# Optimization experiments

Hardware: AMD Instinct MI355X
Metric: run time of the kernel (lower is better)

Reference implementation:

```python
import jax, jax.numpy as jnp
import numpy as np

D_MODEL = 512
NUM_HEADS = 8
D_FF = 2048
SEQ = 2048
BATCH = 2
EPS = 1e-5


def _linear(x, W, b):
    # x: [S,B,D_in], W: [D_out, D_in] (torch convention), b: [D_out]
    return jnp.einsum('sbd,ed->sbe', x, W) + b


def _layer_norm(x, g, b):
    mu = jnp.mean(x, axis=-1, keepdims=True)
    var = jnp.var(x, axis=-1, keepdims=True)
    return (x - mu) * jax.lax.rsqrt(var + EPS) * g + b


def _mha(q_in, k_in, v_in, W, b, mask4d, num_heads):
    # q_in: [Sq,B,D], k_in/v_in: [Sk,B,D]; W: [4,D,D], b: [4,D]
    Sq, B, D = q_in.shape
    Sk = k_in.shape[0]
    dk = D // num_heads
    q = _linear(q_in, W[0], b[0]).reshape(Sq, B, num_heads, dk).transpose(1, 2, 0, 3)
    k = _linear(k_in, W[1], b[1]).reshape(Sk, B, num_heads, dk).transpose(1, 2, 0, 3)
    v = _linear(v_in, W[2], b[2]).reshape(Sk, B, num_heads, dk).transpose(1, 2, 0, 3)
    scores = jnp.einsum('bhqd,bhkd->bhqk', q, k) / jnp.sqrt(jnp.asarray(dk, q.dtype))
    scores = jnp.where(mask4d, -jnp.inf, scores)
    p = jax.nn.softmax(scores, axis=-1)  # dropout p=0 -> identity
    o = jnp.einsum('bhqk,bhkd->bhqd', p, v)  # [B,H,Sq,dk]
    o = o.transpose(2, 0, 1, 3).reshape(Sq, B, D)
    return _linear(o, W[3], b[3])


def setup_inputs() -> dict:
    key = jax.random.key(0)
    ks = jax.random.split(key, 12)
    scale = 1.0 / np.sqrt(D_MODEL)
    inp = {
        'x': jax.random.normal(ks[0], (SEQ, BATCH, D_MODEL), jnp.float32),
        'memory': jax.random.normal(ks[1], (SEQ, BATCH, D_MODEL), jnp.float32),
        # causal mask: True = masked (strictly upper triangular)
        'tgt_mask': jnp.triu(jnp.ones((SEQ, SEQ), dtype=bool), k=1),
        # per-batch key padding mask for cross attention
        'memory_mask': jax.random.randint(ks[2], (BATCH, SEQ), 0, 2) > 0,
        'sa_W': jax.random.normal(ks[3], (4, D_MODEL, D_MODEL), jnp.float32) * scale,
        'sa_b': jnp.zeros((4, D_MODEL), jnp.float32),
        'ca_W': jax.random.normal(ks[4], (4, D_MODEL, D_MODEL), jnp.float32) * scale,
        'ca_b': jnp.zeros((4, D_MODEL), jnp.float32),
        'w1': jax.random.normal(ks[5], (D_FF, D_MODEL), jnp.float32) * scale,
        'b1': jnp.zeros((D_FF,), jnp.float32),
        'w2': jax.random.normal(ks[6], (D_MODEL, D_FF), jnp.float32) * (1.0 / np.sqrt(D_FF)),
        'b2': jnp.zeros((D_MODEL,), jnp.float32),
        'ln_g': jnp.ones((3, D_MODEL), jnp.float32),
        'ln_b': jnp.zeros((3, D_MODEL), jnp.float32),
    }
    return inp


def reference(x, memory, tgt_mask, memory_mask, sa_W, sa_b, ca_W, ca_b,
              w1, b1, w2, b2, ln_g, ln_b):
    # self-attention block (pre-norm, residual)
    nx = _layer_norm(x, ln_g[0], ln_b[0])
    sa = _mha(nx, nx, nx, sa_W, sa_b, tgt_mask[None, None], NUM_HEADS)
    x = x + sa
    # cross-attention block
    nx = _layer_norm(x, ln_g[1], ln_b[1])
    ca = _mha(nx, memory, memory, ca_W, ca_b, memory_mask[:, None, None, :], NUM_HEADS)
    x = x + ca
    # FFN block
    nx = _layer_norm(x, ln_g[2], ln_b[2])
    ff = _linear(jax.nn.relu(_linear(nx, w1, b1)), w2, b2)
    return x + ff
```

## Files before the change

kernel.cpp:

```cpp
#include <hip/hip_runtime.h>

#define S_LEN 2048
#define BATCH_N 2
#define DM 512
#define H_N 8
#define DK_N 64
#define FF_N 2048
#define M_TOK (S_LEN*BATCH_N)
#define QSZ (BATCH_N*H_N*S_LEN*DK_N)
#define MN_PART 2097152

typedef __attribute__((ext_vector_type(8))) short short8;
typedef __attribute__((ext_vector_type(4))) float f32x4;
typedef __attribute__((ext_vector_type(16))) float f32x16;
typedef __attribute__((ext_vector_type(4))) unsigned uint4v;

__device__ __forceinline__ unsigned short f2b(float f) {
  union { float f; unsigned u; } v; v.f = f;
  unsigned r = v.u + 0x7FFFu + ((v.u >> 16) & 1u);
  return (unsigned short)(r >> 16);
}
__device__ __forceinline__ float b2f(unsigned short u) {
  union { unsigned u; float f; } v; v.u = ((unsigned)u) << 16; return v.f;
}

__device__ __forceinline__ void gl_lds16(const void* g, void* l) {
  __builtin_amdgcn_global_load_lds(
      (__attribute__((address_space(1))) unsigned int*)(unsigned long long)g,
      (__attribute__((address_space(3))) unsigned int*)(unsigned int)(unsigned long long)l,
      16, 0, 0);
}

__device__ __forceinline__ void cast4(const float* __restrict__ src,
                                      unsigned short* __restrict__ dst, int i) {
  float4 v = *(const float4*)(src + i);
  ushort4 o; o.x = f2b(v.x); o.y = f2b(v.y); o.z = f2b(v.z); o.w = f2b(v.w);
  *(ushort4*)(dst + i) = o;
}

__device__ __forceinline__ void ln_row_wave(const float* __restrict__ in,
    const float* __restrict__ g, const float* __restrict__ b,
    unsigned short* __restrict__ out, int row, int lane) {
  const float4* src = (const float4*)(in + (size_t)row * DM);
  float4 v0 = src[lane*2], v1 = src[lane*2 + 1];
  float s  = v0.x+v0.y+v0.z+v0.w + v1.x+v1.y+v1.z+v1.w;
  float ss = v0.x*v0.x+v0.y*v0.y+v0.z*v0.z+v0.w*v0.w
           + v1.x*v1.x+v1.y*v1.y+v1.z*v1.z+v1.w*v1.w;
  #pragma unroll
  for (int off = 32; off >= 1; off >>= 1) {
    s  += __shfl_xor(s,  off);
    ss += __shfl_xor(ss, off);
  }
  float mean = s * (1.f/512.f);
  float inv  = rsqrtf(ss * (1.f/512.f) - mean*mean + 1e-5f);
  float4 g0 = ((const float4*)g)[lane*2], g1 = ((const float4*)g)[lane*2 + 1];
  float4 b0 = ((const float4*)b)[lane*2], b1 = ((const float4*)b)[lane*2 + 1];
  ushort4 o0, o1;
  o0.x = f2b((v0.x-mean)*inv*g0.x + b0.x);
  o0.y = f2b((v0.y-mean)*inv*g0.y + b0.y);
  o0.z = f2b((v0.z-mean)*inv*g0.z + b0.z);
  o0.w = f2b((v0.w-mean)*inv*g0.w + b0.w);
  o1.x = f2b((v1.x-mean)*inv*g1.x + b1.x);
  o1.y = f2b((v1.y-mean)*inv*g1.y + b1.y);
  o1.z = f2b((v1.z-mean)*inv*g1.z + b1.z);
  o1.w = f2b((v1.w-mean)*inv*g1.w + b1.w);
  ushort4* dst = (ushort4*)(out + (size_t)row * DM);
  dst[lane*2]     = o0;
  dst[lane*2 + 1] = o1;
}

__global__ __launch_bounds__(256) void prep_kernel(
    const float* __restrict__ sa_W, const float* __restrict__ ca_W,
    const float* __restrict__ w1, const float* __restrict__ w2,
    const float* __restrict__ memory, const int* __restrict__ mm,
    const float* __restrict__ x, const float* __restrict__ ln_g,
    const float* __restrict__ ln_b,
    unsigned short* __restrict__ o_sa, unsigned short* __restrict__ o_ca,
    unsigned short* __restrict__ o_w1, unsigned short* __restrict__ o_w2,
    unsigned short* __restrict__ o_mem, unsigned long long* __restrict__ bmo,
    unsigned short* __restrict__ nx)
{
  int blk = blockIdx.x, t = threadIdx.x;
  if (blk < 1024)      cast4(sa_W, o_sa, (blk*256 + t)*4);
  else if (blk < 2048) cast4(ca_W, o_ca, ((blk-1024)*256 + t)*4);
  else if (blk < 3072) cast4(w1,   o_w1, ((blk-2048)*256 + t)*4);
  else if (blk < 4096) cast4(w2,   o_w2, ((blk-3072)*256 + t)*4);
  else if (blk < 6144) cast4(memory, o_mem, ((blk-4096)*256 + t)*4);
  else if (blk == 6144) {
    if (t < 64) {
      int b = t >> 5, kt = t & 31;
      unsigned long long m = 0ull;
      for (int j = 0; j < 64; j++)
        m |= (unsigned long long)(mm[b*S_LEN + kt*64 + j] != 0) << j;
      bmo[b*32 + kt] = m;
    }
  } else {
    int row = (blk - 6145)*4 + (t >> 6);
    ln_row_wave(x, ln_g, ln_b, nx, row, t & 63);
  }
}

__global__ __launch_bounds__(256) void ln4_kernel(const float* __restrict__ in,
                                                  const float* __restrict__ g,
                                                  const float* __restrict__ b,
                                                  unsigned short* __restrict__ out) {
  ln_row_wave(in, g, b, out, blockIdx.x*4 + (threadIdx.x >> 6), threadIdx.x & 63);
}

template<int RELU, int OUTMODE, int RESID>
__global__ __launch_bounds__(256) void gemm_bt(
    const unsigned short* __restrict__ A, const unsigned short* __restrict__ W,
    const float* __restrict__ bias, const float* __restrict__ resid,
    float* __restrict__ Cf, unsigned short* __restrict__ Cb,
    int M, int N, int K, int Kstride)
{
  __shared__ unsigned short As[2][64*40];
  __shared__ unsigned short Bs[2][64*40];
  int tid = threadIdx.x;
  int lane = tid & 63, w = tid >> 6;
  int wr = w >> 1, wc = w & 1;
  int bm = blockIdx.y * 64, bn = blockIdx.x * 64;
  int kz = blockIdx.z;
  f32x4 acc[2][2] = {};
  int lrow = tid >> 2;
  int lcg  = (tid & 3) * 8;
  const size_t aoff = (size_t)(bm + lrow) * Kstride + (size_t)kz * K + lcg;
  const size_t boff = (size_t)(bn + lrow) * Kstride + (size_t)kz * K + lcg;
  int fr = lane & 15, kg = (lane >> 4) * 8;
  short8 pa = *(const short8*)&A[aoff];
  short8 pb = *(const short8*)&W[boff];
  *(short8*)&As[0][lrow*40 + lcg] = pa;
  *(short8*)&Bs[0][lrow*40 + lcg] = pb;
  __syncthreads();
  int cur = 0;
  for (int k0 = 0; k0 < K; k0 += 32) {
    bool hn = (k0 + 32) < K;
    if (hn) {
      pa = *(const short8*)&A[aoff + k0 + 32];
      pb = *(const short8*)&W[boff + k0 + 32];
    }
    short8 af0 = *(const short8*)&As[cur][(wr*32 +      fr)*40 + kg];
    short8 af1 = *(const short8*)&As[cur][(wr*32 + 16 + fr)*40 + kg];
    short8 bf0 = *(const short8*)&Bs[cur][(wc*32 +      fr)*40 + kg];
    short8 bf1 = *(const short8*)&Bs[cur][(wc*32 + 16 + fr)*40 + kg];
    acc[0][0] = __builtin_amdgcn_mfma_f32_16x16x32_bf16(af0, bf0, acc[0][0], 0,0,0);
    acc[0][1] = __builtin_amdgcn_mfma_f32_16x16x32_bf16(af0, bf1, acc[0][1], 0,0,0);
    acc[1][0] = __builtin_amdgcn_mfma_f32_16x16x32_bf16(af1, bf0, acc[1][0], 0,0,0);
    acc[1][1] = __builtin_amdgcn_mfma_f32_16x16x32_bf16(af1, bf1, acc[1][1], 0,0,0);
    if (hn) {
      *(short8*)&As[cur^1][lrow*40 + lcg] = pa;
      *(short8*)&Bs[cur^1][lrow*40 + lcg] = pb;
    }
    __syncthreads();
    cur ^= 1;
  }
  int rbase = (lane >> 4) * 4;
  #pragma unroll
  for (int m = 0; m < 2; m++) {
    #pragma unroll
    for (int n = 0; n < 2; n++) {
      int col = bn + wc*32 + n*16 + (lane & 15);
      float bc = (OUTMODE == 3) ? 0.f : bias[col];
      #pragma unroll
      for (int r = 0; r < 4; r++) {
        int row = bm + wr*32 + m*16 + rbase + r;
        float vv = acc[m][n][r] + bc;
        if (RELU) vv = fmaxf(vv, 0.f);
        if (OUTMODE == 2) {
          int which = col >> 9, hh = (col >> 6) & 7, dd = col & 63;
          size_t idx = ((((size_t)which*BATCH_N + (row & 1))*H_N + hh)*S_LEN + (row >> 1))*DK_N + dd;
          Cb[idx] = f2b(vv);
        } else if (OUTMODE == 3) {
          Cf[(size_t)kz*MN_PART + (size_t)row*N + col] = vv;
        } else {
          size_t idx = (size_t)row * N + col;
          if (RESID) vv += resid[idx];
          if (OUTMODE == 1) Cb[idx] = f2b(vv);
          else              Cf[idx] = vv;
        }
      }
    }
  }
}

__global__ __launch_bounds__(256) void ffn2_combine(
    const float* __restrict__ part, const float* __restrict__ bias,
    const float* __restrict__ resid, float* __restrict__ out)
{
  int i = (blockIdx.x*256 + threadIdx.x)*4;
  float4 a = *(const float4*)(part + i);
  float4 b = *(const float4*)(part + MN_PART + i);
  float4 c = *(const float4*)(part + 2*MN_PART + i);
  float4 d = *(const float4*)(part + 3*MN_PART + i);
  float4 bs = *(const float4*)(bias + (i & 511));
  float4 rs = *(const float4*)(resid + i);
  float4 o;
  o.x = a.x + b.x + c.x + d.x + bs.x + rs.x;
  o.y = a.y + b.y + c.y + d.y + bs.y + rs.y;
  o.z = a.z + b.z + c.z + d.z + bs.z + rs.z;
  o.w = a.w + b.w + c.w + d.w + bs.w + rs.w;
  *(float4*)(out + i) = o;
}

template<int RELU, int OUTMODE, int VSTART>
__global__ __launch_bounds__(256) void gemm128(
    const unsigned short* __restrict__ A, const unsigned short* __restrict__ W,
    const float* __restrict__ bias, unsigned short* __restrict__ Cb,
    int M, int N, int K)
{
  __shared__ unsigned short As[128*32];
  __shared__ unsigned short Bs[128*32];
  int tid = threadIdx.x, lane = tid & 63, w = tid >> 6;
  int bm = blockIdx.y * 128, bn = blockIdx.x * 128;
  int fr = lane & 15, hi = lane >> 4;
  int kg8 = hi*8, rg = hi*4;
  int wm = (w >> 1) * 64, wn = (w & 1) * 64;
  f32x4 acc[4][4] = {};
  const unsigned short* ga0 = A + (size_t)(bm +      (tid>>2))*K + (tid&3)*8;
  const unsigned short* ga1 = A + (size_t)(bm + 64 + (tid>>2))*K + (tid&3)*8;
  const unsigned short* gb0 = W + (size_t)(bn +      (tid>>2))*K + (tid&3)*8;
  const unsigned short* gb1 = W + (size_t)(bn + 64 + (tid>>2))*K + (tid&3)*8;
  unsigned short* lA0 = &As[tid*8];
  unsigned short* lA1 = &As[2048 + tid*8];
  unsigned short* lB0 = &Bs[tid*8];
  unsigned short* lB1 = &Bs[2048 + tid*8];
  for (int k0 = 0; k0 < K; k0 += 32) {
    gl_lds16(ga0 + k0, lA0);
    gl_lds16(ga1 + k0, lA1);
    gl_lds16(gb0 + k0, lB0);
    gl_lds16(gb1 + k0, lB1);
    __syncthreads();
    short8 af[4], bf[4];
    #pragma unroll
    for (int m = 0; m < 4; m++) af[m] = *(const short8*)&As[(wm + m*16 + fr)*32 + kg8];
    #pragma unroll
    for (int n = 0; n < 4; n++) bf[n] = *(const short8*)&Bs[(wn + n*16 + fr)*32 + kg8];
    __builtin_amdgcn_s_setprio(1);
    #pragma unroll
    for (int m = 0; m < 4; m++)
      #pragma unroll
      for (int n = 0; n < 4; n++)
        acc[m][n] = __builtin_amdgcn_mfma_f32_16x16x32_bf16(af[m], bf[n], acc[m][n], 0,0,0);
    __builtin_amdgcn_s_setprio(0);
    __syncthreads();
  }
  #pragma unroll
  for (int m = 0; m < 4; m++) {
    #pragma unroll
    for (int n = 0; n < 4; n++) {
      int col = bn + wn + n*16 + fr;
      float bc = bias[col];
      #pragma unroll
      for (int r = 0; r < 4; r++) {
        int row = bm + wm + m*16 + rg + r;
        float vv = acc[m][n][r] + bc;
        if (RELU) vv = fmaxf(vv, 0.f);
        if (OUTMODE == 2) {
          int which = col >> 9, hh = (col >> 6) & 7, dd = col & 63;
          int srow = row >> 1, bb = row & 1;
          size_t idx;
          if (which >= VSTART)
            idx = (size_t)which*QSZ + (((size_t)bb*H_N + hh)*DK_N + dd)*S_LEN + srow;
          else
            idx = (size_t)which*QSZ + (((size_t)bb*H_N + hh)*S_LEN + srow)*DK_N + dd;
          Cb[idx] = f2b(vv);
        } else {
          Cb[(size_t)row * N + col] = f2b(vv);
        }
      }
    }
  }
}

__global__ __launch_bounds__(256) void gemm128_dual(
    const unsigned short* __restrict__ A0, const unsigned short* __restrict__ W0,
    const float* __restrict__ bias0, unsigned short* __restrict__ C0,
    const unsigned short* __restrict__ A1, const unsigned short* __restrict__ W1,
    const float* __restrict__ bias1, unsigned short* __restrict__ C1)
{
  const int K = 512;
  int bx = blockIdx.x;
  const unsigned short* A; const unsigned short* W; const float* bias;
  unsigned short* Cb; int bn, vs;
  if (bx < 12) { A = A0; W = W0; bias = bias0; Cb = C0; bn = bx*128;      vs = 2; }
  else         { A = A1; W = W1; bias = bias1; Cb = C1; bn = (bx-12)*128; vs = 1; }
  __shared__ unsigned short As[128*32];
  __shared__ unsigned short Bs[128*32];
  int tid = threadIdx.x, lane = tid & 63, w = tid >> 6;
  int bm = blockIdx.y * 128;
  int fr = lane & 15, hi = lane >> 4;
  int kg8 = hi*8, rg = hi*4;
  int wm = (w >> 1) * 64, wn = (w & 1) * 64;
  f32x4 acc[4][4] = {};
  const unsigned short* ga0 = A + (size_t)(bm +      (tid>>2))*K + (tid&3)*8;
  const unsigned short* ga1 = A + (size_t)(bm + 64 + (tid>>2))*K + (tid&3)*8;
  const unsigned short* gb0 = W + (size_t)(bn +      (tid>>2))*K + (tid&3)*8;
  const unsigned short* gb1 = W + (size_t)(bn + 64 + (tid>>2))*K + (tid&3)*8;
  unsigned short* lA0 = &As[tid*8];
  unsigned short* lA1 = &As[2048 + tid*8];
  unsigned short* lB0 = &Bs[tid*8];
  unsigned short* lB1 = &Bs[2048 + tid*8];
  for (int k0 = 0; k0 < K; k0 += 32) {
    gl_lds16(ga0 + k0, lA0);
    gl_lds16(ga1 + k0, lA1);
    gl_lds16(gb0 + k0, lB0);
    gl_lds16(gb1 + k0, lB1);
    __syncthreads();
    short8 af[4], bf[4];
    #pragma unroll
    for (int m = 0; m < 4; m++) af[m] = *(const short8*)&As[(wm + m*16 + fr)*32 + kg8];
    #pragma unroll
    for (int n = 0; n < 4; n++) bf[n] = *(const short8*)&Bs[(wn + n*16 + fr)*32 + kg8];
    __builtin_amdgcn_s_setprio(1);
    #pragma unroll
    for (int m = 0; m < 4; m++)
      #pragma unroll
      for (int n = 0; n < 4; n++)
        acc[m][n] = __builtin_amdgcn_mfma_f32_16x16x32_bf16(af[m], bf[n], acc[m][n], 0,0,0);
    __builtin_amdgcn_s_setprio(0);
    __syncthreads();
  }
  #pragma unroll
  for (int m = 0; m < 4; m++) {
    #pragma unroll
    for (int n = 0; n < 4; n++) {
      int col = bn + wn + n*16 + fr;
      float bc = bias[col];
      #pragma unroll
      for (int r = 0; r < 4; r++) {
        int row = bm + wm + m*16 + rg + r;
        float vv = acc[m][n][r] + bc;
        int which = col >> 9, hh = (col >> 6) & 7, dd = col & 63;
        int srow = row >> 1, bb = row & 1;
        size_t idx;
        if (which >= vs)
          idx = (size_t)which*QSZ + (((size_t)bb*H_N + hh)*DK_N + dd)*S_LEN + srow;
        else
          idx = (size_t)which*QSZ + (((size_t)bb*H_N + hh)*S_LEN + srow)*DK_N + dd;
        Cb[idx] = f2b(vv);
      }
    }
  }
}

template<int MODE>
__global__ __launch_bounds__(256, 4) void attn3(
    const unsigned short* __restrict__ qg, const unsigned short* __restrict__ kpl,
    const unsigned short* __restrict__ vtpl, const unsigned long long* __restrict__ bm,
    unsigned short* __restrict__ opart, float* __restrict__ lpart)
{
  __shared__ unsigned short SM[2*64*72];
  unsigned short* Ks = SM;
  unsigned short* Vt = SM + 64*72;
  int tid = threadIdx.x;
  int lane = tid & 63, w = tid >> 6;
  int l31 = lane & 31, hi5 = lane >> 5;
  int bid = blockIdx.x;
  int p = bid & 15, u = bid >> 4;
  int qtile = u >> 2, range = u & 3;
  int h = p & 7, b = p >> 3;
  const size_t sbase = (size_t)(b*H_N + h) * S_LEN;
  int kt0 = range*8, kt1 = kt0 + 7;
  if (MODE == 0) {
    int ktmax_tile = qtile*2 + 1;
    if (kt0 > ktmax_tile) {
      int zr = tid >> 1, zc = (tid & 1) * 32;
      short8 z = {};
      size_t zb = (size_t)range*QSZ + (sbase + (size_t)qtile*128 + zr)*DK_N + zc;
      *(short8*)&opart[zb]      = z;
      *(short8*)&opart[zb + 8]  = z;
      *(short8*)&opart[zb + 16] = z;
      *(short8*)&opart[zb + 24] = z;
      if (tid < 128) lpart[range*32768 + (int)sbase + qtile*128 + tid] = 0.f;
      return;
    }
    if (kt1 > ktmax_tile) kt1 = ktmax_tile;
  }
  int qrow = qtile*128 + w*32 + l31;
  short8 qf[4];
  #pragma unroll
  for (int km = 0; km < 4; km++)
    qf[km] = *(const short8*)&qg[(sbase + qrow)*DK_N + km*16 + hi5*8];

  int sr = tid >> 2, sc = (tid & 3) * 16;
  const unsigned short* kbase = &kpl[(sbase + sr)*DK_N + sc];
  const unsigned short* vbase = &vtpl[((size_t)(b*H_N + h)*DK_N + sr)*S_LEN + sc];

  f32x16 oa0 = {}, oa1 = {};
  float lp = 0.f;
  for (int kt = kt0; kt <= kt1; kt++) {
    __syncthreads();
    {
      const unsigned short* kg = kbase + (size_t)kt*64*DK_N;
      const unsigned short* vg = vbase + kt*64;
      *(short8*)&Ks[sr*72 + sc]     = *(const short8*)kg;
      *(short8*)&Ks[sr*72 + sc + 8] = *(const short8*)(kg + 8);
      *(short8*)&Vt[sr*72 + sc]     = *(const short8*)vg;
      *(short8*)&Vt[sr*72 + sc + 8] = *(const short8*)(vg + 8);
    }
    __syncthreads();
    #pragma unroll
    for (int kb = 0; kb < 2; kb++) {
      f32x16 sa = {};
      __builtin_amdgcn_s_setprio(1);
      #pragma unroll
      for (int km = 0; km < 4; km++) {
        short8 kf = *(const short8*)&Ks[(kb*32 + l31)*72 + km*16 + hi5*8];
        sa = __builtin_amdgcn_mfma_f32_32x32x16_bf16(kf, qf[km], sa, 0, 0, 0);
      }
      __builtin_amdgcn_s_setprio(0);
      unsigned mlo = 0;
      if (MODE == 1) mlo = (unsigned)(bm[b*32 + kt] >> (kb*32 + 4*hi5));
      float pv[16];
      float psum = 0.f;
      #pragma unroll
      for (int r = 0; r < 16; r++) {
        const int pos = (r & 3) + 8*(r >> 2);
        float e = __expf(sa[r] * 0.125f);
        bool dead;
        if (MODE == 0) dead = (kt*64 + kb*32 + 4*hi5 + pos) > qrow;
        else           dead = ((mlo >> pos) & 1u) != 0u;
        e = dead ? 0.f : e;
        pv[r] = e;
        psum += e;
      }
      lp += psum;
      unsigned pk[8];
      #pragma unroll
      for (int i = 0; i < 8; i++)
        asm("v_cvt_pk_bf16_f32 %0, %1, %2" : "=v"(pk[i]) : "v"(pv[2*i]), "v"(pv[2*i+1]));
      asm("v_permlane32_swap_b32 %0, %1" : "+v"(pk[0]), "+v"(pk[2]));
      asm("v_permlane32_swap_b32 %0, %1" : "+v"(pk[1]), "+v"(pk[3]));
      asm("v_permlane32_swap_b32 %0, %1" : "+v"(pk[4]), "+v"(pk[6]));
      asm("v_permlane32_swap_b32 %0, %1" : "+v"(pk[5]), "+v"(pk[7]));
      uint4v f0v, f1v;
      f0v.x = pk[0]; f0v.y = pk[1]; f0v.z = pk[2]; f0v.w = pk[3];
      f1v.x = pk[4]; f1v.y = pk[5]; f1v.z = pk[6]; f1v.w = pk[7];
      short8 pf0 = *(short8*)&f0v;
      short8 pf1 = *(short8*)&f1v;
      __builtin_amdgcn_s_setprio(1);
      {
        short8 v00 = *(const short8*)&Vt[(     l31)*72 + kb*32 +      hi5*8];
        short8 v01 = *(const short8*)&Vt[(     l31)*72 + kb*32 + 16 + hi5*8];
        oa0 = __builtin_amdgcn_mfma_f32_32x32x16_bf16(pf0, v00, oa0, 0, 0, 0);
        oa0 = __builtin_amdgcn_mfma_f32_32x32x16_bf16(pf1, v01, oa0, 0, 0, 0);
        short8 v10 = *(const short8*)&Vt[(32 + l31)*72 + kb*32 +      hi5*8];
        short8 v11 = *(const short8*)&Vt[(32 + l31)*72 + kb*32 + 16 + hi5*8];
        oa1 = __builtin_amdgcn_mfma_f32_32x32x16_bf16(pf0, v10, oa1, 0, 0, 0);
        oa1 = __builtin_amdgcn_mfma_f32_32x32x16_bf16(pf1, v11, oa1, 0, 0, 0);
      }
      __builtin_amdgcn_s_setprio(0);
    }
  }
  float lptot = lp + __shfl_xor(lp, 32);
  if (lane < 32)
    lpart[range*32768 + (int)sbase + qtile*128 + w*32 + l31] = lptot;
  #pragma unroll
  for (int r = 0; r < 16; r++) {
    const int pos = (r & 3) + 8*(r >> 2);
    int qr = qtile*128 + w*32 + pos + 4*hi5;
    size_t obase = (size_t)range*QSZ + (sbase + (size_t)qr)*DK_N;
    opart[obase + l31]      = f2b(oa0[r]);
    opart[obase + 32 + l31] = f2b(oa1[r]);
  }
}

__global__ __launch_bounds__(256) void attn_combine4(
    const unsigned short* __restrict__ op, const float* __restrict__ lp,
    unsigned short* __restrict__ o)
{
  int t = blockIdx.x*256 + threadIdx.x;
  int f = t*8;
  int col = f & 511, row = f >> 9;
  int h = col >> 6, d = col & 63, s = row >> 1, b = row & 1;
  size_t pr = ((size_t)b*H_N + h)*S_LEN + s;
  size_t base = pr*DK_N + d;
  float acc[8] = {0.f,0.f,0.f,0.f,0.f,0.f,0.f,0.f};
  float l = 0.f;
  #pragma unroll
  for (int r = 0; r < 4; r++) {
    short8 a = *(const short8*)&op[(size_t)r*QSZ + base];
    #pragma unroll
    for (int i = 0; i < 8; i++) acc[i] += b2f((unsigned short)a[i]);
    l += lp[r*32768 + (int)pr];
  }
  float inv = 1.f / l;
  short8 r8;
  #pragma unroll
  for (int i = 0; i < 8; i++) r8[i] = (short)f2b(acc[i] * inv);
  *(short8*)&o[(size_t)row*DM + col] = r8;
}

extern "C" void kernel_launch(void* const* d_in, const int* in_sizes, int n_in,
                              void* d_out, int out_size, void* d_ws, size_t ws_size,
                              hipStream_t stream) {
  const float* x       = (const float*)d_in[0];
  const float* memory  = (const float*)d_in[1];
  const int*   memmask = (const int*)d_in[3];
  const float* sa_W = (const float*)d_in[4];
  const float* sa_b = (const float*)d_in[5];
  const float* ca_W = (const float*)d_in[6];
  const float* ca_b = (const float*)d_in[7];
  const float* w1   = (const float*)d_in[8];
  const float* b1   = (const float*)d_in[9];
  const float* w2   = (const float*)d_in[10];
  const float* b2   = (const float*)d_in[11];
  const float* ln_g = (const float*)d_in[12];
  const float* ln_b = (const float*)d_in[13];
  float* out = (float*)d_out;

  char* ws = (char*)d_ws;
  float*          xcur   = (float*)ws;
  unsigned short* nx_bf  = (unsigned short*)(ws + (8u<<20));
  unsigned short* qkv_sa = (unsigned short*)(ws + (12u<<20));
  unsigned short* q_ca   = (unsigned short*)(ws + (24u<<20));
  unsigned short* kv_ca  = (unsigned short*)(ws + (28u<<20));
  unsigned short* o_bf   = (unsigned short*)(ws + (36u<<20));
  unsigned short* mem_bf = (unsigned short*)(ws + (40u<<20));
  unsigned short* h_bf   = (unsigned short*)(ws + (44u<<20));
  unsigned short* opart  = (unsigned short*)(ws + (44u<<20));
  float*          fpart  = (float*)(ws + (12u<<20));
  float*          lpart  = (float*)(ws + (60u<<20));
  unsigned long long* bmsk = (unsigned long long*)(ws + (60u<<20) + (1u<<19));
  unsigned short* w_sa   = (unsigned short*)(ws + (61u<<20));
  unsigned short* w_ca   = w_sa + 4*512*512;
  unsigned short* w_f1   = w_ca + 4*512*512;
  unsigned short* w_f2   = w_f1 + 2048*512;

  dim3 blk(256);
  dim3 g512 (512/64,  4096/64);
  dim3 gdual(20, 4096/128);
  dim3 q128_2048(2048/128, 4096/128);
  dim3 gsplitk(512/64, 4096/64, 4);

  prep_kernel<<<7169, blk, 0, stream>>>(sa_W, ca_W, w1, w2, memory, memmask,
                                        x, ln_g, ln_b,
                                        w_sa, w_ca, w_f1, w_f2, mem_bf, bmsk, nx_bf);

  gemm128_dual<<<gdual, blk, 0, stream>>>(nx_bf, w_sa, sa_b, qkv_sa,
                                          mem_bf, w_ca + 262144, ca_b + 512, kv_ca);
  attn3<0><<<1024, blk, 0, stream>>>(qkv_sa, qkv_sa + QSZ, qkv_sa + 2*QSZ, nullptr, opart, lpart);
  attn_combine4<<<1024, blk, 0, stream>>>(opart, lpart, o_bf);
  gemm_bt<0,0,1><<<g512, blk, 0, stream>>>(o_bf, w_sa + 3*262144, sa_b + 1536, x, xcur, nullptr, 4096, 512, 512, 512);

  ln4_kernel<<<1024, blk, 0, stream>>>(xcur, ln_g + 512, ln_b + 512, nx_bf);
  gemm_bt<0,2,0><<<g512, blk, 0, stream>>>(nx_bf, w_ca, ca_b, nullptr, nullptr, q_ca, 4096, 512, 512, 512);
  attn3<1><<<1024, blk, 0, stream>>>(q_ca, kv_ca, kv_ca + QSZ, bmsk, opart, lpart);
  attn_combine4<<<1024, blk, 0, stream>>>(opart, lpart, o_bf);
  gemm_bt<0,0,1><<<g512, blk, 0, stream>>>(o_bf, w_ca + 3*262144, ca_b + 1536, xcur, xcur, nullptr, 4096, 512, 512, 512);

  ln4_kernel<<<1024, blk, 0, stream>>>(xcur, ln_g + 1024, ln_b + 1024, nx_bf);
  gemm128<1,1,0><<<q128_2048, blk, 0, stream>>>(nx_bf, w_f1, b1, h_bf, 4096, 2048, 512);
  gemm_bt<0,3,0><<<gsplitk, blk, 0, stream>>>(h_bf, w_f2, nullptr, nullptr, fpart, nullptr, 4096, 512, 512, 2048);
  ffn2_combine<<<2048, blk, 0, stream>>>(fpart, b2, xcur, out);
}
```

Baseline: 201.6 us.

## Fuse attention split combine into output projection and trim causal work

Removes the attn_combine4 kernels. The output-projection GEMM now reads the bf16 split partials and row sums directly and normalizes them while loading its A tiles, and for causal attention it only reads the splits that are active. The softmax scale moves into the Q projection epilogue. Causal attention no longer writes zero partials for fully masked tiles, skips key tiles past each wave's diagonal, and applies the mask only on the diagonal tile. FFN2 split-K drops from 4 to 2 with a lighter combine. In exchange, each projection block redoes the combine on every A load, which adds global reads and ALU work inside the GEMM loop, and the partial-sum layout changes.

```diff
diff --git a/kernel.cpp b/kernel.cpp
--- a/kernel.cpp
+++ b/kernel.cpp
@@ -107,12 +107,47 @@
   ln_row_wave(in, g, b, out, blockIdx.x*4 + (threadIdx.x >> 6), threadIdx.x & 63);
 }
 
-template<int RELU, int OUTMODE, int RESID>
+template<int CAUSAL>
+__device__ __forceinline__ short8 comb8(const unsigned short* __restrict__ op,
+                                        const float* __restrict__ lp,
+                                        int arow, int col) {
+  int s = arow >> 1, bb = arow & 1;
+  int h = col >> 6, d = col & 63;
+  int pr = (bb*H_N + h)*S_LEN + s;
+  size_t pbase = (size_t)pr*DK_N + d;
+  int nact = CAUSAL ? ((s >> 9) + 1) : 4;
+  float4 lv = *(const float4*)(lp + (size_t)pr*4);
+  float ls;
+  if (CAUSAL) {
+    ls = lv.x;
+    if (nact > 1) ls += lv.y;
+    if (nact > 2) ls += lv.z;
+    if (nact > 3) ls += lv.w;
+  } else {
+    ls = lv.x + lv.y + lv.z + lv.w;
+  }
+  float inv = 1.f / ls;
+  float a[8] = {0.f,0.f,0.f,0.f,0.f,0.f,0.f,0.f};
+  #pragma unroll
+  for (int r = 0; r < 4; r++) {
+    if (!CAUSAL || r < nact) {
+      short8 t = *(const short8*)&op[(size_t)r*QSZ + pbase];
+      #pragma unroll
+      for (int i = 0; i < 8; i++) a[i] += b2f((unsigned short)t[i]);
+    }
+  }
+  short8 o;
+  #pragma unroll
+  for (int i = 0; i < 8; i++) o[i] = (short)f2b(a[i]*inv);
+  return o;
+}
+
+template<int RELU, int OUTMODE, int RESID, int ACOMB>
 __global__ __launch_bounds__(256) void gemm_bt(
     const unsigned short* __restrict__ A, const unsigned short* __restrict__ W,
     const float* __restrict__ bias, const float* __restrict__ resid,
     float* __restrict__ Cf, unsigned short* __restrict__ Cb,
-    int M, int N, int K, int Kstride)
+    int M, int N, int K, int Kstride, const float* __restrict__ lp)
 {
   __shared__ unsigned short As[2][64*40];
   __shared__ unsigned short Bs[2][64*40];
@@ -127,8 +162,10 @@
   const size_t aoff = (size_t)(bm + lrow) * Kstride + (size_t)kz * K + lcg;
   const size_t boff = (size_t)(bn + lrow) * Kstride + (size_t)kz * K + lcg;
   int fr = lane & 15, kg = (lane >> 4) * 8;
-  short8 pa = *(const short8*)&A[aoff];
-  short8 pb = *(const short8*)&W[boff];
+  short8 pa, pb;
+  if (ACOMB) pa = comb8<ACOMB==2>(A, lp, bm + lrow, lcg);
+  else       pa = *(const short8*)&A[aoff];
+  pb = *(const short8*)&W[boff];
   *(short8*)&As[0][lrow*40 + lcg] = pa;
   *(short8*)&Bs[0][lrow*40 + lcg] = pb;
   __syncthreads();
@@ -136,7 +173,8 @@
   for (int k0 = 0; k0 < K; k0 += 32) {
     bool hn = (k0 + 32) < K;
     if (hn) {
-      pa = *(const short8*)&A[aoff + k0 + 32];
+      if (ACOMB) pa = comb8<ACOMB==2>(A, lp, bm + lrow, k0 + 32 + lcg);
+      else       pa = *(const short8*)&A[aoff + k0 + 32];
       pb = *(const short8*)&W[boff + k0 + 32];
     }
     short8 af0 = *(const short8*)&As[cur][(wr*32 +      fr)*40 + kg];
@@ -168,6 +206,7 @@
         if (RELU) vv = fmaxf(vv, 0.f);
         if (OUTMODE == 2) {
           int which = col >> 9, hh = (col >> 6) & 7, dd = col & 63;
+          if (which == 0) vv *= 0.125f;
           size_t idx = ((((size_t)which*BATCH_N + (row & 1))*H_N + hh)*S_LEN + (row >> 1))*DK_N + dd;
           Cb[idx] = f2b(vv);
         } else if (OUTMODE == 3) {
@@ -190,15 +229,13 @@
   int i = (blockIdx.x*256 + threadIdx.x)*4;
   float4 a = *(const float4*)(part + i);
   float4 b = *(const float4*)(part + MN_PART + i);
-  float4 c = *(const float4*)(part + 2*MN_PART + i);
-  float4 d = *(const float4*)(part + 3*MN_PART + i);
   float4 bs = *(const float4*)(bias + (i & 511));
   float4 rs = *(const float4*)(resid + i);
   float4 o;
-  o.x = a.x + b.x + c.x + d.x + bs.x + rs.x;
-  o.y = a.y + b.y + c.y + d.y + bs.y + rs.y;
-  o.z = a.z + b.z + c.z + d.z + bs.z + rs.z;
-  o.w = a.w + b.w + c.w + d.w + bs.w + rs.w;
+  o.x = a.x + b.x + bs.x + rs.x;
+  o.y = a.y + b.y + bs.y + rs.y;
+  o.z = a.z + b.z + bs.z + rs.z;
+  o.w = a.w + b.w + bs.w + rs.w;
   *(float4*)(out + i) = o;
 }
 
@@ -331,6 +368,7 @@
         int row = bm + wm + m*16 + rg + r;
         float vv = acc[m][n][r] + bc;
         int which = col >> 9, hh = (col >> 6) & 7, dd = col & 63;
+        if (vs == 2 && which == 0) vv *= 0.125f;
         int srow = row >> 1, bb = row & 1;
         size_t idx;
         if (which >= vs)
@@ -362,21 +400,12 @@
   const size_t sbase = (size_t)(b*H_N + h) * S_LEN;
   int kt0 = range*8, kt1 = kt0 + 7;
   if (MODE == 0) {
-    int ktmax_tile = qtile*2 + 1;
-    if (kt0 > ktmax_tile) {
-      int zr = tid >> 1, zc = (tid & 1) * 32;
-      short8 z = {};
-      size_t zb = (size_t)range*QSZ + (sbase + (size_t)qtile*128 + zr)*DK_N + zc;
-      *(short8*)&opart[zb]      = z;
-      *(short8*)&opart[zb + 8]  = z;
-      *(short8*)&opart[zb + 16] = z;
-      *(short8*)&opart[zb + 24] = z;
-      if (tid < 128) lpart[range*32768 + (int)sbase + qtile*128 + tid] = 0.f;
-      return;
-    }
-    if (kt1 > ktmax_tile) kt1 = ktmax_tile;
-  }
-  int qrow = qtile*128 + w*32 + l31;
+    if (kt0 > qtile*2 + 1) return;
+    if (kt1 > qtile*2 + 1) kt1 = qtile*2 + 1;
+  }
+  int wbase = qtile*128 + w*32;
+  int ktw = (wbase + 31) >> 6;
+  int qrow = wbase + l31;
   short8 qf[4];
   #pragma unroll
   for (int km = 0; km < 4; km++)
@@ -399,6 +428,8 @@
       *(short8*)&Vt[sr*72 + sc + 8] = *(const short8*)(vg + 8);
     }
     __syncthreads();
+    if (MODE == 0 && kt > ktw) continue;
+    bool dmask = (MODE == 0) && (kt == ktw);
     #pragma unroll
     for (int kb = 0; kb < 2; kb++) {
       f32x16 sa = {};
@@ -409,20 +440,31 @@
         sa = __builtin_amdgcn_mfma_f32_32x32x16_bf16(kf, qf[km], sa, 0, 0, 0);
       }
       __builtin_amdgcn_s_setprio(0);
-      unsigned mlo = 0;
-      if (MODE == 1) mlo = (unsigned)(bm[b*32 + kt] >> (kb*32 + 4*hi5));
       float pv[16];
       float psum = 0.f;
-      #pragma unroll
-      for (int r = 0; r < 16; r++) {
-        const int pos = (r & 3) + 8*(r >> 2);
-        float e = __expf(sa[r] * 0.125f);
-        bool dead;
-        if (MODE == 0) dead = (kt*64 + kb*32 + 4*hi5 + pos) > qrow;
-        else           dead = ((mlo >> pos) & 1u) != 0u;
-        e = dead ? 0.f : e;
-        pv[r] = e;
-        psum += e;
+      if (MODE == 1) {
+        unsigned mlo = (unsigned)(bm[b*32 + kt] >> (kb*32 + 4*hi5));
+        #pragma unroll
+        for (int r = 0; r < 16; r++) {
+          const int pos = (r & 3) + 8*(r >> 2);
+          float e = __expf(sa[r]);
+          if ((mlo >> pos) & 1u) e = 0.f;
+          pv[r] = e; psum += e;
+        }
+      } else if (dmask) {
+        #pragma unroll
+        for (int r = 0; r < 16; r++) {
+          const int pos = (r & 3) + 8*(r >> 2);
+          float e = __expf(sa[r]);
+          if (kt*64 + kb*32 + 4*hi5 + pos > qrow) e = 0.f;
+          pv[r] = e; psum += e;
+        }
+      } else {
+        #pragma unroll
+        for (int r = 0; r < 16; r++) {
+          float e = __expf(sa[r]);
+          pv[r] = e; psum += e;
+        }
       }
       lp += psum;
       unsigned pk[8];
@@ -454,41 +496,15 @@
   }
   float lptot = lp + __shfl_xor(lp, 32);
   if (lane < 32)
-    lpart[range*32768 + (int)sbase + qtile*128 + w*32 + l31] = lptot;
+    lpart[((size_t)sbase + wbase + l31)*4 + range] = lptot;
   #pragma unroll
   for (int r = 0; r < 16; r++) {
     const int pos = (r & 3) + 8*(r >> 2);
-    int qr = qtile*128 + w*32 + pos + 4*hi5;
+    int qr = wbase + pos + 4*hi5;
     size_t obase = (size_t)range*QSZ + (sbase + (size_t)qr)*DK_N;
     opart[obase + l31]      = f2b(oa0[r]);
     opart[obase + 32 + l31] = f2b(oa1[r]);
   }
-}
-
-__global__ __launch_bounds__(256) void attn_combine4(
-    const unsigned short* __restrict__ op, const float* __restrict__ lp,
-    unsigned short* __restrict__ o)
-{
-  int t = blockIdx.x*256 + threadIdx.x;
-  int f = t*8;
-  int col = f & 511, row = f >> 9;
-  int h = col >> 6, d = col & 63, s = row >> 1, b = row & 1;
-  size_t pr = ((size_t)b*H_N + h)*S_LEN + s;
-  size_t base = pr*DK_N + d;
-  float acc[8] = {0.f,0.f,0.f,0.f,0.f,0.f,0.f,0.f};
-  float l = 0.f;
-  #pragma unroll
-  for (int r = 0; r < 4; r++) {
-    short8 a = *(const short8*)&op[(size_t)r*QSZ + base];
-    #pragma unroll
-    for (int i = 0; i < 8; i++) acc[i] += b2f((unsigned short)a[i]);
-    l += lp[r*32768 + (int)pr];
-  }
-  float inv = 1.f / l;
-  short8 r8;
-  #pragma unroll
-  for (int i = 0; i < 8; i++) r8[i] = (short)f2b(acc[i] * inv);
-  *(short8*)&o[(size_t)row*DM + col] = r8;
 }
 
 extern "C" void kernel_launch(void* const* d_in, const int* in_sizes, int n_in,
@@ -515,7 +531,6 @@
   unsigned short* qkv_sa = (unsigned short*)(ws + (12u<<20));
   unsigned short* q_ca   = (unsigned short*)(ws + (24u<<20));
   unsigned short* kv_ca  = (unsigned short*)(ws + (28u<<20));
-  unsigned short* o_bf   = (unsigned short*)(ws + (36u<<20));
   unsigned short* mem_bf = (unsigned short*)(ws + (40u<<20));
   unsigned short* h_bf   = (unsigned short*)(ws + (44u<<20));
   unsigned short* opart  = (unsigned short*)(ws + (44u<<20));
@@ -531,7 +546,7 @@
   dim3 g512 (512/64,  4096/64);
   dim3 gdual(20, 4096/128);
   dim3 q128_2048(2048/128, 4096/128);
-  dim3 gsplitk(512/64, 4096/64, 4);
+  dim3 gsplitk(512/64, 4096/64, 2);
 
   prep_kernel<<<7169, blk, 0, stream>>>(sa_W, ca_W, w1, w2, memory, memmask,
                                         x, ln_g, ln_b,
@@ -540,17 +555,15 @@
   gemm128_dual<<<gdual, blk, 0, stream>>>(nx_bf, w_sa, sa_b, qkv_sa,
                                           mem_bf, w_ca + 262144, ca_b + 512, kv_ca);
   attn3<0><<<1024, blk, 0, stream>>>(qkv_sa, qkv_sa + QSZ, qkv_sa + 2*QSZ, nullptr, opart, lpart);
-  attn_combine4<<<1024, blk, 0, stream>>>(opart, lpart, o_bf);
-  gemm_bt<0,0,1><<<g512, blk, 0, stream>>>(o_bf, w_sa + 3*262144, sa_b + 1536, x, xcur, nullptr, 4096, 512, 512, 512);
+  gemm_bt<0,0,1,2><<<g512, blk, 0, stream>>>(opart, w_sa + 3*262144, sa_b + 1536, x, xcur, nullptr, 4096, 512, 512, 512, lpart);
 
   ln4_kernel<<<1024, blk, 0, stream>>>(xcur, ln_g + 512, ln_b + 512, nx_bf);
-  gemm_bt<0,2,0><<<g512, blk, 0, stream>>>(nx_bf, w_ca, ca_b, nullptr, nullptr, q_ca, 4096, 512, 512, 512);
+  gemm_bt<0,2,0,0><<<g512, blk, 0, stream>>>(nx_bf, w_ca, ca_b, nullptr, nullptr, q_ca, 4096, 512, 512, 512, nullptr);
   attn3<1><<<1024, blk, 0, stream>>>(q_ca, kv_ca, kv_ca + QSZ, bmsk, opart, lpart);
-  attn_combine4<<<1024, blk, 0, stream>>>(opart, lpart, o_bf);
-  gemm_bt<0,0,1><<<g512, blk, 0, stream>>>(o_bf, w_ca + 3*262144, ca_b + 1536, xcur, xcur, nullptr, 4096, 512, 512, 512);
+  gemm_bt<0,0,1,1><<<g512, blk, 0, stream>>>(opart, w_ca + 3*262144, ca_b + 1536, xcur, xcur, nullptr, 4096, 512, 512, 512, lpart);
 
   ln4_kernel<<<1024, blk, 0, stream>>>(xcur, ln_g + 1024, ln_b + 1024, nx_bf);
   gemm128<1,1,0><<<q128_2048, blk, 0, stream>>>(nx_bf, w_f1, b1, h_bf, 4096, 2048, 512);
-  gemm_bt<0,3,0><<<gsplitk, blk, 0, stream>>>(h_bf, w_f2, nullptr, nullptr, fpart, nullptr, 4096, 512, 512, 2048);
+  gemm_bt<0,3,0,0><<<gsplitk, blk, 0, stream>>>(h_bf, w_f2, nullptr, nullptr, fpart, nullptr, 4096, 512, 1024, 2048, nullptr);
   ffn2_combine<<<2048, blk, 0, stream>>>(fpart, b2, xcur, out);
 }
```

Measured after the change: 213.8 us. 1.06x slower.
